# Optimization experiments

Hardware: AMD Instinct MI355X
Metric: run time of the kernel (lower is better)

Reference implementation:

```python
import jax, jax.numpy as jnp
import numpy as np

B, S, D, H = 4, 2048, 1024, 16
DK = D // H


def setup_inputs() -> dict:
    key = jax.random.key(0)
    ks = jax.random.split(key, 11)
    scale = 1.0 / np.sqrt(D)
    inp = {
        "query": jax.random.normal(ks[0], (B, S, D), jnp.float32),
        "key": jax.random.normal(ks[1], (B, S, D), jnp.float32),
        "value": jax.random.normal(ks[2], (B, S, D), jnp.float32),
    }
    # 4 linear layers: Wq, Wk, Wv, Wo (torch Linear: y = x @ W.T + b)
    for i, name in enumerate(["q", "k", "v", "o"]):
        inp[f"W{name}"] = jax.random.uniform(ks[3 + 2 * i], (D, D), jnp.float32, -scale, scale)
        inp[f"b{name}"] = jax.random.uniform(ks[4 + 2 * i], (D,), jnp.float32, -scale, scale)
    return inp


def reference(query, key, value, Wq, bq, Wk, bk, Wv, bv, Wo, bo):
    def proj(x, W, b):
        # [B,S,D] -> [B,H,S,DK]
        y = x @ W.T + b
        return y.reshape(B, S, H, DK).transpose(0, 2, 1, 3)

    q = proj(query, Wq, bq)
    k = proj(key, Wk, bk)
    v = proj(value, Wv, bv)
    scores = jnp.einsum("bhqd,bhkd->bhqk", q, k) / jnp.sqrt(jnp.float32(DK))
    p = jax.nn.softmax(scores, axis=-1)  # dropout p=0 -> identity
    ctx = jnp.einsum("bhqk,bhkd->bhqd", p, v)
    ctx = ctx.transpose(0, 2, 1, 3).reshape(B, S, D)
    return ctx @ Wo.T + bo
```

## Files before the change

### kernel.cpp

```cpp
#include <hip/hip_runtime.h>

typedef unsigned short u16;
typedef unsigned int u32;
typedef __attribute__((ext_vector_type(8))) short short8v;
typedef __attribute__((ext_vector_type(4))) float floatx4;

#define BB 4
#define SS 2048
#define DD 1024
#define HH 16
#define DKK 64
#define MM (BB * SS)
#define KK DD
#define NN DD
#define QSCALE 0.18033688011112042f

__device__ __forceinline__ u16 f2bf(float f) {
  union { __bf16 h; u16 u; } r; r.h = (__bf16)f; return r.u;
}
__device__ __forceinline__ u32 pack2bf(float a, float b) {
  union { u32 u; __bf16 h[2]; } r;
  r.h[0] = (__bf16)a; r.h[1] = (__bf16)b; return r.u;
}

__device__ __forceinline__ void load_lds16(const void* g, void* l) {
  __builtin_amdgcn_global_load_lds((const __attribute__((address_space(1))) void*)g,
                                   (__attribute__((address_space(3))) void*)l, 16, 0, 0);
}

__device__ __forceinline__ floatx4 mfma_k32(short8v a, short8v b, floatx4 c) {
  return __builtin_amdgcn_mfma_f32_16x16x32_bf16(a, b, c, 0, 0, 0);
}

__global__ __launch_bounds__(256) void cvt_w4(const float* __restrict__ w0,
                                              const float* __restrict__ w1,
                                              const float* __restrict__ w2,
                                              const float* __restrict__ w3,
                                              u16* __restrict__ out) {
  const int y = blockIdx.y;
  const float* in = (y == 0) ? w0 : (y == 1) ? w1 : (y == 2) ? w2 : w3;
  u16* o = out + (size_t)y * DD * DD;
  const int i = (blockIdx.x * 256 + threadIdx.x) * 8;
  float4 a = *(const float4*)(in + i);
  float4 b = *(const float4*)(in + i + 4);
  uint4 v;
  v.x = pack2bf(a.x, a.y); v.y = pack2bf(a.z, a.w);
  v.z = pack2bf(b.x, b.y); v.w = pack2bf(b.z, b.w);
  *(uint4*)(o + i) = v;
}

__global__ __launch_bounds__(256) void cvt_a3(const float* __restrict__ a0,
                                              const float* __restrict__ a1,
                                              const float* __restrict__ a2,
                                              u16* __restrict__ o0, u16* __restrict__ o1,
                                              u16* __restrict__ o2) {
  const int y = blockIdx.y;
  const float* in = (y == 0) ? a0 : (y == 1) ? a1 : a2;
  u16* o = (y == 0) ? o0 : (y == 1) ? o1 : o2;
  const int i = (blockIdx.x * 256 + threadIdx.x) * 8;
  float4 a = *(const float4*)(in + i);
  float4 b = *(const float4*)(in + i + 4);
  uint4 v;
  v.x = pack2bf(a.x, a.y); v.y = pack2bf(a.z, a.w);
  v.z = pack2bf(b.x, b.y); v.w = pack2bf(b.z, b.w);
  *(uint4*)(o + i) = v;
}

#define NT (KK / 64)
#define ITERS (NT / 2)

__device__ __forceinline__ void stage_half(const u16* __restrict__ gsrc, u16* ldst,
                                           int tid) {
#pragma unroll
  for (int L = 0; L < 2; ++L) {
    const int s = L * 512 + tid;
    const int r = s >> 3;
    const int g = (s & 7) ^ (r & 7);
    load_lds16(gsrc + (size_t)r * KK + g * 8, ldst + s * 8);
  }
}

__device__ __forceinline__ void gemm256_core(const u16* __restrict__ A,
                                             const u16* __restrict__ W,
                                             u16* As, u16* Bs,
                                             floatx4 (&acc)[8][4]) {
  const int tid = threadIdx.x;
  const int w = tid >> 6, lane = tid & 63;
  const int wm = w >> 2, wn = w & 3;
  const int wnh = wn >> 1, wno = wn & 1;
  const int lr = lane & 15;
  const int c0 = (((lane >> 2) & 1) << 5) | ((((lane >> 4) ^ lane) & 3) << 3);

#define AP(d, fr, kk) \
  (*(const short8v*)(As + ((d)*2 + wm) * 8192 + ((fr)*16 + lr) * 64 + (c0 ^ ((kk)*32))))
#define BP(d, fc, kk) \
  (*(const short8v*)(Bs + ((d)*2 + wnh) * 8192 + (wno * 64 + (fc)*16 + lr) * 64 + (c0 ^ ((kk)*32))))
#define MFMA8(FROFF, B, FCOFF)                                                  \
  _Pragma("unroll") for (int fr_ = 0; fr_ < 4; ++fr_)                           \
  _Pragma("unroll") for (int fc_ = 0; fc_ < 2; ++fc_) {                         \
    acc[(FROFF) + fr_][(FCOFF) + fc_] =                                         \
        mfma_k32(a[fr_][0], B[fc_][0], acc[(FROFF) + fr_][(FCOFF) + fc_]);      \
    acc[(FROFF) + fr_][(FCOFF) + fc_] =                                         \
        mfma_k32(a[fr_][1], B[fc_][1], acc[(FROFF) + fr_][(FCOFF) + fc_]);      \
  }
#define BAR() __builtin_amdgcn_s_barrier()
#define PRIO1() __builtin_amdgcn_s_setprio(1)
#define PRIO0() __builtin_amdgcn_s_setprio(0)

  short8v a[4][2], b01[2][2], b23[2][2];

  stage_half(A, As + 0 * 8192, tid);
  stage_half(A + (size_t)128 * KK, As + 1 * 8192, tid);
  stage_half(W, Bs + 0 * 8192, tid);
  stage_half(W + (size_t)128 * KK, Bs + 1 * 8192, tid);
  stage_half(W + 64, Bs + 2 * 8192, tid);
  stage_half(W + (size_t)128 * KK + 64, Bs + 3 * 8192, tid);
  asm volatile("s_waitcnt vmcnt(4)" ::: "memory");
  BAR();

#pragma unroll 1
  for (int j = 0; j < ITERS; ++j) {
    const int e = 2 * j, o = e + 1;
    const bool haveE2 = (j + 1 < ITERS);
#pragma unroll
    for (int fr = 0; fr < 4; ++fr) { a[fr][0] = AP(0, fr, 0); a[fr][1] = AP(0, fr, 1); }
#pragma unroll
    for (int fc = 0; fc < 2; ++fc) { b01[fc][0] = BP(0, fc, 0); b01[fc][1] = BP(0, fc, 1); }
    stage_half(A + (size_t)o * 64, As + 2 * 8192, tid);
    BAR(); PRIO1(); MFMA8(0, b01, 0); PRIO0(); BAR();
#pragma unroll
    for (int fc = 0; fc < 2; ++fc) { b23[fc][0] = BP(0, fc + 2, 0); b23[fc][1] = BP(0, fc + 2, 1); }
    stage_half(A + (size_t)128 * KK + (size_t)o * 64, As + 3 * 8192, tid);
    BAR(); PRIO1(); MFMA8(0, b23, 2); PRIO0(); BAR();
#pragma unroll
    for (int fr = 0; fr < 4; ++fr) { a[fr][0] = AP(0, fr + 4, 0); a[fr][1] = AP(0, fr + 4, 1); }
    if (haveE2) stage_half(W + (size_t)(e + 2) * 64, Bs + 0 * 8192, tid);
    BAR(); PRIO1(); MFMA8(4, b01, 0); PRIO0(); BAR();
    if (haveE2) {
      stage_half(W + (size_t)128 * KK + (size_t)(e + 2) * 64, Bs + 1 * 8192, tid);
      asm volatile("s_waitcnt vmcnt(4)" ::: "memory");
    } else {
      asm volatile("s_waitcnt vmcnt(0)" ::: "memory");
    }
    BAR(); PRIO1(); MFMA8(4, b23, 2); PRIO0(); BAR();
#pragma unroll
    for (int fr = 0; fr < 4; ++fr) { a[fr][0] = AP(1, fr, 0); a[fr][1] = AP(1, fr, 1); }
#pragma unroll
    for (int fc = 0; fc < 2; ++fc) { b01[fc][0] = BP(1, fc, 0); b01[fc][1] = BP(1, fc, 1); }
    if (haveE2) stage_half(A + (size_t)(e + 2) * 64, As + 0 * 8192, tid);
    BAR(); PRIO1(); MFMA8(0, b01, 0); PRIO0(); BAR();
#pragma unroll
    for (int fc = 0; fc < 2; ++fc) { b23[fc][0] = BP(1, fc + 2, 0); b23[fc][1] = BP(1, fc + 2, 1); }
    if (haveE2) stage_half(A + (size_t)128 * KK + (size_t)(e + 2) * 64, As + 1 * 8192, tid);
    BAR(); PRIO1(); MFMA8(0, b23, 2); PRIO0(); BAR();
#pragma unroll
    for (int fr = 0; fr < 4; ++fr) { a[fr][0] = AP(1, fr + 4, 0); a[fr][1] = AP(1, fr + 4, 1); }
    if (haveE2) stage_half(W + (size_t)(o + 2) * 64, Bs + 2 * 8192, tid);
    BAR(); PRIO1(); MFMA8(4, b01, 0); PRIO0(); BAR();
    if (haveE2) {
      stage_half(W + (size_t)128 * KK + (size_t)(o + 2) * 64, Bs + 3 * 8192, tid);
      asm volatile("s_waitcnt vmcnt(4)" ::: "memory");
    }
    BAR(); PRIO1(); MFMA8(4, b23, 2); PRIO0(); BAR();
  }
#undef AP
#undef BP
#undef MFMA8
#undef BAR
#undef PRIO1
#undef PRIO0
}

__global__ __launch_bounds__(512, 2) void proj_gemm(
    const u16* __restrict__ qc, const u16* __restrict__ kc, const u16* __restrict__ vc,
    const u16* __restrict__ Wq, const u16* __restrict__ Wk, const u16* __restrict__ Wv,
    const float* __restrict__ bq, const float* __restrict__ bk, const float* __restrict__ bv,
    u16* __restrict__ Qb, u16* __restrict__ Kb, u16* __restrict__ Vtb) {
  __shared__ __align__(16) u16 As[2 * 2 * 8192];
  __shared__ __align__(16) u16 Bs[2 * 2 * 8192];
  const int z = blockIdx.z;
  const u16* A = (z == 0) ? qc : (z == 1) ? kc : vc;
  const u16* W = (z == 0) ? Wq : (z == 1) ? Wk : Wv;
  const float* bias = (z == 0) ? bq : (z == 1) ? bk : bv;
  const int m0 = blockIdx.x * 256, n0 = blockIdx.y * 256;

  floatx4 acc[8][4] = {};
  gemm256_core(A + (size_t)m0 * KK, W + (size_t)n0 * KK, As, Bs, acc);

  const int tid = threadIdx.x;
  const int w = tid >> 6, lane = tid & 63;
  const int lr = lane & 15, lq = lane >> 4;
  const int wm = w >> 2, wn = w & 3;
  const int row0 = m0 + wm * 128;
  const int col0 = n0 + wn * 64;

  if (z == 2) {
#pragma unroll
    for (int fc = 0; fc < 4; ++fc) {
      const int col = col0 + fc * 16 + lr;
      const float bv_ = bias[col];
      const int h = col >> 6, dk = col & 63;
#pragma unroll
      for (int fr = 0; fr < 8; ++fr) {
        const int row = row0 + fr * 16 + lq * 4;
        const int b = row >> 11, s = row & (SS - 1);
        const int kt = s >> 6, key = s & 63;
        uint2 pk;
        pk.x = pack2bf(acc[fr][fc][0] + bv_, acc[fr][fc][1] + bv_);
        pk.y = pack2bf(acc[fr][fc][2] + bv_, acc[fr][fc][3] + bv_);
        const size_t addr = (((size_t)(b * HH + h)) * 32 + kt) * 4096 +
                            1024 * (dk >> 4) + 512 * (key >> 5) +
                            128 * ((key >> 2) & 3) + 8 * (dk & 15) +
                            ((key >> 4) & 1) * 4;
        *(uint2*)&Vtb[addr] = pk;
      }
    }
  } else {
    u16* out = (z == 0) ? Qb : Kb;
    const float sc = (z == 0) ? QSCALE : 1.0f;
#pragma unroll
    for (int fc = 0; fc < 4; ++fc) {
      const int col = col0 + fc * 16 + lr;
      const float bv_ = bias[col];
#pragma unroll
      for (int fr = 0; fr < 8; ++fr)
#pragma unroll
        for (int rr = 0; rr < 4; ++rr) {
          const int row = row0 + fr * 16 + lq * 4 + rr;
          out[(size_t)row * NN + col] = f2bf((acc[fr][fc][rr] + bv_) * sc);
        }
    }
  }
}

__global__ __launch_bounds__(512, 2) void out_gemm(const u16* __restrict__ A,
                                                   const u16* __restrict__ W,
                                                   const float* __restrict__ bias,
                                                   float* __restrict__ out) {
  __shared__ __align__(16) u16 As[2 * 2 * 8192];
  __shared__ __align__(16) u16 Bs[2 * 2 * 8192];
  const int m0 = blockIdx.x * 256, n0 = blockIdx.y * 256;
  floatx4 acc[8][4] = {};
  gemm256_core(A + (size_t)m0 * KK, W + (size_t)n0 * KK, As, Bs, acc);

  const int tid = threadIdx.x;
  const int w = tid >> 6, lane = tid & 63;
  const int lr = lane & 15, lq = lane >> 4;
  const int wm = w >> 2, wn = w & 3;
  const int row0 = m0 + wm * 128;
  const int col0 = n0 + wn * 64;
#pragma unroll
  for (int fc = 0; fc < 4; ++fc) {
    const int col = col0 + fc * 16 + lr;
    const float bv = bias[col];
#pragma unroll
    for (int fr = 0; fr < 8; ++fr)
#pragma unroll
      for (int rr = 0; rr < 4; ++rr) {
        const int row = row0 + fr * 16 + lq * 4 + rr;
        out[(size_t)row * NN + col] = acc[fr][fc][rr] + bv;
      }
  }
}

__global__ __launch_bounds__(256, 4) void attn_kernel(const u16* __restrict__ Q,
                                                      const u16* __restrict__ Kmat,
                                                      const u16* __restrict__ Vt,
                                                      u16* __restrict__ ctx) {
  __shared__ __align__(16) u16 Ks[2][64 * 64];
  __shared__ __align__(16) u16 Vs[2][64 * 64];
  const int tid = threadIdx.x;
  const int w = tid >> 6, lane = tid & 63;
  const int lr = lane & 15, lq = lane >> 4;
  const int bh = blockIdx.x, b = bh >> 4, h = bh & 15;
  const int q0 = blockIdx.y * 128;

  short8v qf[2][2];
  {
    const u16* qp = Q + ((size_t)(b * SS + q0 + w * 32 + lr)) * DD + h * 64 + lq * 8;
    qf[0][0] = *(const short8v*)qp;
    qf[0][1] = *(const short8v*)(qp + 32);
    qf[1][0] = *(const short8v*)(qp + 16 * DD);
    qf[1][1] = *(const short8v*)(qp + 16 * DD + 32);
  }
  floatx4 o[2][4] = {};
  float l_part[2] = {};

  const u16* kp = Kmat + ((size_t)(b * SS + w * 16 + lr)) * DD + h * 64 + lq * 8;
  const u16* vp = Vt + ((size_t)(b * HH + h)) * (32 * 4096) + (2 * w) * 512 + lane * 8;

  load_lds16(kp,       &Ks[0][(2 * w) * 512]);
  load_lds16(kp + 32,  &Ks[0][(2 * w + 1) * 512]);
  load_lds16(vp,       &Vs[0][(2 * w) * 512]);
  load_lds16(vp + 512, &Vs[0][(2 * w + 1) * 512]);
  kp += 64 * DD; vp += 4096;

#pragma unroll 1
  for (int kt = 0; kt < SS / 64; ++kt) {
    const int bf = kt & 1;
    const bool haveNext = (kt + 1 < SS / 64);
    __builtin_amdgcn_s_barrier();
    if (haveNext) {
      load_lds16(kp,       &Ks[bf ^ 1][(2 * w) * 512]);
      load_lds16(kp + 32,  &Ks[bf ^ 1][(2 * w + 1) * 512]);
      load_lds16(vp,       &Vs[bf ^ 1][(2 * w) * 512]);
      load_lds16(vp + 512, &Vs[bf ^ 1][(2 * w + 1) * 512]);
      kp += 64 * DD; vp += 4096;
      asm volatile("s_waitcnt vmcnt(4)" ::: "memory");
    } else {
      asm volatile("s_waitcnt vmcnt(0)" ::: "memory");
    }
    __builtin_amdgcn_s_barrier();

    floatx4 sc[2][4] = {};
    __builtin_amdgcn_s_setprio(1);
#pragma unroll
    for (int t = 0; t < 4; ++t) {
      short8v kb0 = *(const short8v*)&Ks[bf][t * 1024 + lane * 8];
      short8v kb1 = *(const short8v*)&Ks[bf][t * 1024 + 512 + lane * 8];
#pragma unroll
      for (int s = 0; s < 2; ++s) {
        sc[s][t] = mfma_k32(kb0, qf[s][0], sc[s][t]);
        sc[s][t] = mfma_k32(kb1, qf[s][1], sc[s][t]);
      }
    }
    __builtin_amdgcn_s_setprio(0);

    short8v pa[2][2];
#pragma unroll
    for (int s = 0; s < 2; ++s) {
      float lp = 0.0f;
#pragma unroll
      for (int t = 0; t < 4; ++t)
#pragma unroll
        for (int r = 0; r < 4; ++r) {
          const float e = __builtin_amdgcn_exp2f(sc[s][t][r]);
          sc[s][t][r] = e;
          lp += e;
        }
      l_part[s] += lp;
#pragma unroll
      for (int H = 0; H < 2; ++H) {
        union { u32 u[4]; short8v v; } pb;
        pb.u[0] = pack2bf(sc[s][2 * H][0], sc[s][2 * H][1]);
        pb.u[1] = pack2bf(sc[s][2 * H][2], sc[s][2 * H][3]);
        pb.u[2] = pack2bf(sc[s][2 * H + 1][0], sc[s][2 * H + 1][1]);
        pb.u[3] = pack2bf(sc[s][2 * H + 1][2], sc[s][2 * H + 1][3]);
        pa[s][H] = pb.v;
      }
    }

    const u16* vsb = &Vs[bf][0];
    __builtin_amdgcn_s_setprio(1);
#pragma unroll
    for (int t = 0; t < 4; ++t) {
      short8v vb0 = *(const short8v*)&vsb[(2 * t) * 512 + lane * 8];
      short8v vb1 = *(const short8v*)&vsb[(2 * t + 1) * 512 + lane * 8];
#pragma unroll
      for (int s = 0; s < 2; ++s) {
        o[s][t] = mfma_k32(pa[s][0], vb0, o[s][t]);
        o[s][t] = mfma_k32(pa[s][1], vb1, o[s][t]);
      }
    }
    __builtin_amdgcn_s_setprio(0);
  }

  float inv[2][4];
#pragma unroll
  for (int s = 0; s < 2; ++s) {
    float l = l_part[s];
    l += __shfl_xor(l, 16);
    l += __shfl_xor(l, 32);
#pragma unroll
    for (int r = 0; r < 4; ++r)
      inv[s][r] = 1.0f / __shfl(l, lq * 4 + r);
  }

#pragma unroll
  for (int s = 0; s < 2; ++s)
#pragma unroll
    for (int r = 0; r < 4; ++r) {
      const int sq = q0 + w * 32 + s * 16 + lq * 4 + r;
      u16* cp = ctx + ((size_t)(b * SS + sq)) * DD + h * 64;
      const float iv = inv[s][r];
#pragma unroll
      for (int t = 0; t < 4; ++t)
        cp[t * 16 + lr] = f2bf(o[s][t][r] * iv);
    }
}

extern "C" void kernel_launch(void* const* d_in, const int* in_sizes, int n_in,
                              void* d_out, int out_size, void* d_ws, size_t ws_size,
                              hipStream_t stream) {
  const float* query = (const float*)d_in[0];
  const float* key   = (const float*)d_in[1];
  const float* value = (const float*)d_in[2];
  const float* Wq = (const float*)d_in[3];  const float* bq = (const float*)d_in[4];
  const float* Wk = (const float*)d_in[5];  const float* bk = (const float*)d_in[6];
  const float* Wv = (const float*)d_in[7];  const float* bv = (const float*)d_in[8];
  const float* Wo = (const float*)d_in[9];  const float* bo = (const float*)d_in[10];
  float* out = (float*)d_out;

  char* ws = (char*)d_ws;
  size_t off = 0;
  u16* Wb   = (u16*)(ws + off); off += (size_t)4 * DD * DD * 2;
  u16* Qb   = (u16*)(ws + off); off += (size_t)MM * DD * 2;
  u16* Kb   = (u16*)(ws + off); off += (size_t)MM * DD * 2;
  u16* Vtb  = (u16*)(ws + off); off += (size_t)MM * DD * 2;
  u16* qc   = (u16*)(ws + off);
  u16* ctxb = qc;               off += (size_t)MM * DD * 2;
  u16* kc = (u16*)d_out;
  u16* vc = (u16*)d_out + (size_t)MM * DD;
  u16* Wq_b = Wb, *Wk_b = Wb + (size_t)DD * DD, *Wv_b = Wb + (size_t)2 * DD * DD,
     *Wo_b = Wb + (size_t)3 * DD * DD;

  const int wn = DD * DD, an = MM * DD;
  cvt_w4<<<dim3(wn / 2048, 4), 256, 0, stream>>>(Wq, Wk, Wv, Wo, Wb);
  cvt_a3<<<dim3(an / 2048, 3), 256, 0, stream>>>(query, key, value, qc, kc, vc);

  proj_gemm<<<dim3(MM / 256, NN / 256, 3), 512, 0, stream>>>(
      qc, kc, vc, Wq_b, Wk_b, Wv_b, bq, bk, bv, Qb, Kb, Vtb);

  attn_kernel<<<dim3(BB * HH, SS / 128), 256, 0, stream>>>(Qb, Kb, Vtb, ctxb);

  out_gemm<<<dim3(MM / 256, NN / 256), 512, 0, stream>>>(ctxb, Wo_b, bo, out);
}
```

Baseline: 345.3 us.

## Software-pipeline attention loop: overlap next QK^T with previous PV

Restructures the attention inner loop so that each iteration computes QK^T for tile kt and then P·V for tile kt-1, with the softmax of tile kt deferred to the end of the iteration. V gets a triple buffer in LDS, and there is a prologue (first QK plus softmax) and an epilogue (last PV). The aim is to keep the MFMA pipe busy across the exp/pack dependency chain instead of stalling between the QK, softmax and PV phases. It uses more LDS and keeps extra registers (pa) live across iterations, which may lower occupancy.

```diff
diff --git a/kernel.cpp b/kernel.cpp
--- a/kernel.cpp
+++ b/kernel.cpp
@@ -267,8 +267,8 @@
                                                       const u16* __restrict__ Kmat,
                                                       const u16* __restrict__ Vt,
                                                       u16* __restrict__ ctx) {
-  __shared__ __align__(16) u16 Ks[2][64 * 64];
-  __shared__ __align__(16) u16 Vs[2][64 * 64];
+  __shared__ __align__(16) u16 Ks[2][4096];
+  __shared__ __align__(16) u16 Vs[3][4096];
   const int tid = threadIdx.x;
   const int w = tid >> 6, lane = tid & 63;
   const int lr = lane & 15, lq = lane >> 4;
@@ -285,26 +285,80 @@
   }
   floatx4 o[2][4] = {};
   float l_part[2] = {};
+  short8v pa[2][2];
 
   const u16* kp = Kmat + ((size_t)(b * SS + w * 16 + lr)) * DD + h * 64 + lq * 8;
   const u16* vp = Vt + ((size_t)(b * HH + h)) * (32 * 4096) + (2 * w) * 512 + lane * 8;
+
+#define QK_BLOCK(KSB)                                                        \
+  _Pragma("unroll") for (int t = 0; t < 4; ++t) {                            \
+    short8v kb0 = *(const short8v*)&(KSB)[t * 1024 + lane * 8];              \
+    short8v kb1 = *(const short8v*)&(KSB)[t * 1024 + 512 + lane * 8];        \
+    _Pragma("unroll") for (int s = 0; s < 2; ++s) {                          \
+      sc[s][t] = mfma_k32(kb0, qf[s][0], sc[s][t]);                          \
+      sc[s][t] = mfma_k32(kb1, qf[s][1], sc[s][t]);                          \
+    }                                                                        \
+  }
+#define PV_BLOCK(VSB)                                                        \
+  _Pragma("unroll") for (int t = 0; t < 4; ++t) {                            \
+    short8v vb0 = *(const short8v*)&(VSB)[(2 * t) * 512 + lane * 8];         \
+    short8v vb1 = *(const short8v*)&(VSB)[(2 * t + 1) * 512 + lane * 8];     \
+    _Pragma("unroll") for (int s = 0; s < 2; ++s) {                          \
+      o[s][t] = mfma_k32(pa[s][0], vb0, o[s][t]);                            \
+      o[s][t] = mfma_k32(pa[s][1], vb1, o[s][t]);                            \
+    }                                                                        \
+  }
+#define SM_BLOCK()                                                           \
+  _Pragma("unroll") for (int s = 0; s < 2; ++s) {                            \
+    float lp = 0.0f;                                                         \
+    _Pragma("unroll") for (int t = 0; t < 4; ++t)                            \
+      _Pragma("unroll") for (int r = 0; r < 4; ++r) {                        \
+        const float e = __builtin_amdgcn_exp2f(sc[s][t][r]);                 \
+        sc[s][t][r] = e;                                                     \
+        lp += e;                                                             \
+      }                                                                      \
+    l_part[s] += lp;                                                         \
+    _Pragma("unroll") for (int H = 0; H < 2; ++H) {                          \
+      union { u32 u[4]; short8v v; } pb;                                     \
+      pb.u[0] = pack2bf(sc[s][2 * H][0], sc[s][2 * H][1]);                   \
+      pb.u[1] = pack2bf(sc[s][2 * H][2], sc[s][2 * H][3]);                   \
+      pb.u[2] = pack2bf(sc[s][2 * H + 1][0], sc[s][2 * H + 1][1]);           \
+      pb.u[3] = pack2bf(sc[s][2 * H + 1][2], sc[s][2 * H + 1][3]);           \
+      pa[s][H] = pb.v;                                                       \
+    }                                                                        \
+  }
 
   load_lds16(kp,       &Ks[0][(2 * w) * 512]);
   load_lds16(kp + 32,  &Ks[0][(2 * w + 1) * 512]);
   load_lds16(vp,       &Vs[0][(2 * w) * 512]);
   load_lds16(vp + 512, &Vs[0][(2 * w + 1) * 512]);
   kp += 64 * DD; vp += 4096;
-
+  load_lds16(kp,       &Ks[1][(2 * w) * 512]);
+  load_lds16(kp + 32,  &Ks[1][(2 * w + 1) * 512]);
+  load_lds16(vp,       &Vs[1][(2 * w) * 512]);
+  load_lds16(vp + 512, &Vs[1][(2 * w + 1) * 512]);
+  kp += 64 * DD; vp += 4096;
+  asm volatile("s_waitcnt vmcnt(4)" ::: "memory");
+  __builtin_amdgcn_s_barrier();
+
+  {
+    floatx4 sc[2][4] = {};
+    __builtin_amdgcn_s_setprio(1);
+    QK_BLOCK(Ks[0])
+    __builtin_amdgcn_s_setprio(0);
+    SM_BLOCK()
+  }
+
+  int vprev = 0, vcur = 1, vnxt = 2;
 #pragma unroll 1
-  for (int kt = 0; kt < SS / 64; ++kt) {
-    const int bf = kt & 1;
+  for (int kt = 1; kt < SS / 64; ++kt) {
     const bool haveNext = (kt + 1 < SS / 64);
     __builtin_amdgcn_s_barrier();
     if (haveNext) {
-      load_lds16(kp,       &Ks[bf ^ 1][(2 * w) * 512]);
-      load_lds16(kp + 32,  &Ks[bf ^ 1][(2 * w + 1) * 512]);
-      load_lds16(vp,       &Vs[bf ^ 1][(2 * w) * 512]);
-      load_lds16(vp + 512, &Vs[bf ^ 1][(2 * w + 1) * 512]);
+      load_lds16(kp,       &Ks[(kt + 1) & 1][(2 * w) * 512]);
+      load_lds16(kp + 32,  &Ks[(kt + 1) & 1][(2 * w + 1) * 512]);
+      load_lds16(vp,       &Vs[vnxt][(2 * w) * 512]);
+      load_lds16(vp + 512, &Vs[vnxt][(2 * w + 1) * 512]);
       kp += 64 * DD; vp += 4096;
       asm volatile("s_waitcnt vmcnt(4)" ::: "memory");
     } else {
@@ -313,57 +367,26 @@
     __builtin_amdgcn_s_barrier();
 
     floatx4 sc[2][4] = {};
+    const u16* ksb = &Ks[kt & 1][0];
+    const u16* vsb = &Vs[vprev][0];
     __builtin_amdgcn_s_setprio(1);
-#pragma unroll
-    for (int t = 0; t < 4; ++t) {
-      short8v kb0 = *(const short8v*)&Ks[bf][t * 1024 + lane * 8];
-      short8v kb1 = *(const short8v*)&Ks[bf][t * 1024 + 512 + lane * 8];
-#pragma unroll
-      for (int s = 0; s < 2; ++s) {
-        sc[s][t] = mfma_k32(kb0, qf[s][0], sc[s][t]);
-        sc[s][t] = mfma_k32(kb1, qf[s][1], sc[s][t]);
-      }
-    }
+    QK_BLOCK(ksb)
+    PV_BLOCK(vsb)
     __builtin_amdgcn_s_setprio(0);
-
-    short8v pa[2][2];
-#pragma unroll
-    for (int s = 0; s < 2; ++s) {
-      float lp = 0.0f;
-#pragma unroll
-      for (int t = 0; t < 4; ++t)
-#pragma unroll
-        for (int r = 0; r < 4; ++r) {
-          const float e = __builtin_amdgcn_exp2f(sc[s][t][r]);
-          sc[s][t][r] = e;
-          lp += e;
-        }
-      l_part[s] += lp;
-#pragma unroll
-      for (int H = 0; H < 2; ++H) {
-        union { u32 u[4]; short8v v; } pb;
-        pb.u[0] = pack2bf(sc[s][2 * H][0], sc[s][2 * H][1]);
-        pb.u[1] = pack2bf(sc[s][2 * H][2], sc[s][2 * H][3]);
-        pb.u[2] = pack2bf(sc[s][2 * H + 1][0], sc[s][2 * H + 1][1]);
-        pb.u[3] = pack2bf(sc[s][2 * H + 1][2], sc[s][2 * H + 1][3]);
-        pa[s][H] = pb.v;
-      }
-    }
-
-    const u16* vsb = &Vs[bf][0];
+    SM_BLOCK()
+
+    vprev = vcur; vcur = vnxt; vnxt = (vnxt + 1 == 3) ? 0 : vnxt + 1;
+  }
+
+  {
+    const u16* vsb = &Vs[vprev][0];
     __builtin_amdgcn_s_setprio(1);
-#pragma unroll
-    for (int t = 0; t < 4; ++t) {
-      short8v vb0 = *(const short8v*)&vsb[(2 * t) * 512 + lane * 8];
-      short8v vb1 = *(const short8v*)&vsb[(2 * t + 1) * 512 + lane * 8];
-#pragma unroll
-      for (int s = 0; s < 2; ++s) {
-        o[s][t] = mfma_k32(pa[s][0], vb0, o[s][t]);
-        o[s][t] = mfma_k32(pa[s][1], vb1, o[s][t]);
-      }
-    }
+    PV_BLOCK(vsb)
     __builtin_amdgcn_s_setprio(0);
   }
+#undef QK_BLOCK
+#undef PV_BLOCK
+#undef SM_BLOCK
 
   float inv[2][4];
 #pragma unroll
```

Result: no change. 345.1 us (-0.1%).

## Split attention block into 8 waves of 16 query rows, MFMA row-sum

Applied to the files above, without the earlier changes.

The attention kernel now uses 512 threads (8 waves), each owning 16 query rows instead of 32. Each wave issues half as many K/V tile loads and a single MFMA set per tile. The softmax denominator is now computed with an extra MFMA against a ones vector, replacing the scalar exp-sum and cross-lane shuffles. The aim is more waves per CU for latency hiding, fewer registers per wave, and less VALU work. In exchange each wave reuses every K/V LDS read for fewer rows and does two extra MFMAs per tile.

```diff
diff --git a/kernel.cpp b/kernel.cpp
--- a/kernel.cpp
+++ b/kernel.cpp
@@ -263,36 +263,40 @@
   }
 }
 
-__global__ __launch_bounds__(256, 4) void attn_kernel(const u16* __restrict__ Q,
+__global__ __launch_bounds__(512, 8) void attn_kernel(const u16* __restrict__ Q,
                                                       const u16* __restrict__ Kmat,
                                                       const u16* __restrict__ Vt,
                                                       u16* __restrict__ ctx) {
-  __shared__ __align__(16) u16 Ks[2][64 * 64];
-  __shared__ __align__(16) u16 Vs[2][64 * 64];
+  __shared__ __align__(16) u16 Ks[2][4096];
+  __shared__ __align__(16) u16 Vs[2][4096];
   const int tid = threadIdx.x;
   const int w = tid >> 6, lane = tid & 63;
   const int lr = lane & 15, lq = lane >> 4;
   const int bh = blockIdx.x, b = bh >> 4, h = bh & 15;
   const int q0 = blockIdx.y * 128;
 
-  short8v qf[2][2];
+  short8v qf[2];
   {
-    const u16* qp = Q + ((size_t)(b * SS + q0 + w * 32 + lr)) * DD + h * 64 + lq * 8;
-    qf[0][0] = *(const short8v*)qp;
-    qf[0][1] = *(const short8v*)(qp + 32);
-    qf[1][0] = *(const short8v*)(qp + 16 * DD);
-    qf[1][1] = *(const short8v*)(qp + 16 * DD + 32);
-  }
-  floatx4 o[2][4] = {};
-  float l_part[2] = {};
-
-  const u16* kp = Kmat + ((size_t)(b * SS + w * 16 + lr)) * DD + h * 64 + lq * 8;
-  const u16* vp = Vt + ((size_t)(b * HH + h)) * (32 * 4096) + (2 * w) * 512 + lane * 8;
-
-  load_lds16(kp,       &Ks[0][(2 * w) * 512]);
-  load_lds16(kp + 32,  &Ks[0][(2 * w + 1) * 512]);
-  load_lds16(vp,       &Vs[0][(2 * w) * 512]);
-  load_lds16(vp + 512, &Vs[0][(2 * w + 1) * 512]);
+    const u16* qp = Q + ((size_t)(b * SS + q0 + w * 16 + lr)) * DD + h * 64 + lq * 8;
+    qf[0] = *(const short8v*)qp;
+    qf[1] = *(const short8v*)(qp + 32);
+  }
+  short8v ones;
+  {
+    union { u16 u[8]; short8v v; } ob;
+#pragma unroll
+    for (int i = 0; i < 8; ++i) ob.u[i] = 0x3F80;
+    ones = ob.v;
+  }
+  floatx4 o[4] = {};
+  floatx4 acc_l = {};
+
+  const u16* kp = Kmat + ((size_t)(b * SS + (w >> 1) * 16 + lr)) * DD + h * 64 +
+                  (w & 1) * 32 + lq * 8;
+  const u16* vp = Vt + ((size_t)(b * HH + h)) * (32 * 4096) + w * 512 + lane * 8;
+
+  load_lds16(kp, &Ks[0][w * 512]);
+  load_lds16(vp, &Vs[0][w * 512]);
   kp += 64 * DD; vp += 4096;
 
 #pragma unroll 1
@@ -301,53 +305,40 @@
     const bool haveNext = (kt + 1 < SS / 64);
     __builtin_amdgcn_s_barrier();
     if (haveNext) {
-      load_lds16(kp,       &Ks[bf ^ 1][(2 * w) * 512]);
-      load_lds16(kp + 32,  &Ks[bf ^ 1][(2 * w + 1) * 512]);
-      load_lds16(vp,       &Vs[bf ^ 1][(2 * w) * 512]);
-      load_lds16(vp + 512, &Vs[bf ^ 1][(2 * w + 1) * 512]);
+      load_lds16(kp, &Ks[bf ^ 1][w * 512]);
+      load_lds16(vp, &Vs[bf ^ 1][w * 512]);
       kp += 64 * DD; vp += 4096;
-      asm volatile("s_waitcnt vmcnt(4)" ::: "memory");
+      asm volatile("s_waitcnt vmcnt(2)" ::: "memory");
     } else {
       asm volatile("s_waitcnt vmcnt(0)" ::: "memory");
     }
     __builtin_amdgcn_s_barrier();
 
-    floatx4 sc[2][4] = {};
+    floatx4 sc[4] = {};
     __builtin_amdgcn_s_setprio(1);
 #pragma unroll
     for (int t = 0; t < 4; ++t) {
       short8v kb0 = *(const short8v*)&Ks[bf][t * 1024 + lane * 8];
       short8v kb1 = *(const short8v*)&Ks[bf][t * 1024 + 512 + lane * 8];
-#pragma unroll
-      for (int s = 0; s < 2; ++s) {
-        sc[s][t] = mfma_k32(kb0, qf[s][0], sc[s][t]);
-        sc[s][t] = mfma_k32(kb1, qf[s][1], sc[s][t]);
-      }
+      sc[t] = mfma_k32(kb0, qf[0], sc[t]);
+      sc[t] = mfma_k32(kb1, qf[1], sc[t]);
     }
     __builtin_amdgcn_s_setprio(0);
 
-    short8v pa[2][2];
-#pragma unroll
-    for (int s = 0; s < 2; ++s) {
-      float lp = 0.0f;
-#pragma unroll
-      for (int t = 0; t < 4; ++t)
-#pragma unroll
-        for (int r = 0; r < 4; ++r) {
-          const float e = __builtin_amdgcn_exp2f(sc[s][t][r]);
-          sc[s][t][r] = e;
-          lp += e;
-        }
-      l_part[s] += lp;
-#pragma unroll
-      for (int H = 0; H < 2; ++H) {
-        union { u32 u[4]; short8v v; } pb;
-        pb.u[0] = pack2bf(sc[s][2 * H][0], sc[s][2 * H][1]);
-        pb.u[1] = pack2bf(sc[s][2 * H][2], sc[s][2 * H][3]);
-        pb.u[2] = pack2bf(sc[s][2 * H + 1][0], sc[s][2 * H + 1][1]);
-        pb.u[3] = pack2bf(sc[s][2 * H + 1][2], sc[s][2 * H + 1][3]);
-        pa[s][H] = pb.v;
-      }
+    short8v pa[2];
+#pragma unroll
+    for (int t = 0; t < 4; ++t)
+#pragma unroll
+      for (int r = 0; r < 4; ++r)
+        sc[t][r] = __builtin_amdgcn_exp2f(sc[t][r]);
+#pragma unroll
+    for (int H = 0; H < 2; ++H) {
+      union { u32 u[4]; short8v v; } pb;
+      pb.u[0] = pack2bf(sc[2 * H][0], sc[2 * H][1]);
+      pb.u[1] = pack2bf(sc[2 * H][2], sc[2 * H][3]);
+      pb.u[2] = pack2bf(sc[2 * H + 1][0], sc[2 * H + 1][1]);
+      pb.u[3] = pack2bf(sc[2 * H + 1][2], sc[2 * H + 1][3]);
+      pa[H] = pb.v;
     }
 
     const u16* vsb = &Vs[bf][0];
@@ -356,37 +347,23 @@
     for (int t = 0; t < 4; ++t) {
       short8v vb0 = *(const short8v*)&vsb[(2 * t) * 512 + lane * 8];
       short8v vb1 = *(const short8v*)&vsb[(2 * t + 1) * 512 + lane * 8];
-#pragma unroll
-      for (int s = 0; s < 2; ++s) {
-        o[s][t] = mfma_k32(pa[s][0], vb0, o[s][t]);
-        o[s][t] = mfma_k32(pa[s][1], vb1, o[s][t]);
-      }
-    }
+      o[t] = mfma_k32(pa[0], vb0, o[t]);
+      o[t] = mfma_k32(pa[1], vb1, o[t]);
+    }
+    acc_l = mfma_k32(pa[0], ones, acc_l);
+    acc_l = mfma_k32(pa[1], ones, acc_l);
     __builtin_amdgcn_s_setprio(0);
   }
 
-  float inv[2][4];
-#pragma unroll
-  for (int s = 0; s < 2; ++s) {
-    float l = l_part[s];
-    l += __shfl_xor(l, 16);
-    l += __shfl_xor(l, 32);
-#pragma unroll
-    for (int r = 0; r < 4; ++r)
-      inv[s][r] = 1.0f / __shfl(l, lq * 4 + r);
-  }
-
-#pragma unroll
-  for (int s = 0; s < 2; ++s)
-#pragma unroll
-    for (int r = 0; r < 4; ++r) {
-      const int sq = q0 + w * 32 + s * 16 + lq * 4 + r;
-      u16* cp = ctx + ((size_t)(b * SS + sq)) * DD + h * 64;
-      const float iv = inv[s][r];
-#pragma unroll
-      for (int t = 0; t < 4; ++t)
-        cp[t * 16 + lr] = f2bf(o[s][t][r] * iv);
-    }
+#pragma unroll
+  for (int r = 0; r < 4; ++r) {
+    const int sq = q0 + w * 16 + lq * 4 + r;
+    u16* cp = ctx + ((size_t)(b * SS + sq)) * DD + h * 64;
+    const float iv = 1.0f / acc_l[r];
+#pragma unroll
+    for (int t = 0; t < 4; ++t)
+      cp[t * 16 + lr] = f2bf(o[t][r] * iv);
+  }
 }
 
 extern "C" void kernel_launch(void* const* d_in, const int* in_sizes, int n_in,
@@ -421,7 +398,7 @@
   proj_gemm<<<dim3(MM / 256, NN / 256, 3), 512, 0, stream>>>(
       qc, kc, vc, Wq_b, Wk_b, Wv_b, bq, bk, bv, Qb, Kb, Vtb);
 
-  attn_kernel<<<dim3(BB * HH, SS / 128), 256, 0, stream>>>(Qb, Kb, Vtb, ctxb);
+  attn_kernel<<<dim3(BB * HH, SS / 128), 512, 0, stream>>>(Qb, Kb, Vtb, ctxb);
 
   out_gemm<<<dim3(MM / 256, NN / 256), 512, 0, stream>>>(ctxb, Wo_b, bo, out);
 }
```

Result: no change. 343.7 us (-0.5%).
